# Kernel tuning notes

Hardware: AMD Instinct MI355X
Metric: run time of the kernel (lower is better)

The kernel has to match this reference:

```python
import jax, jax.numpy as jnp
import numpy as np

N, DIM, NH, HD, M = 2048, 1024, 16, 64, 2
LN_EPS = 1e-5


def setup_inputs() -> dict:
    key = jax.random.key(0)
    ks = jax.random.split(key, 8)
    x = jax.random.normal(ks[0], (N, DIM), dtype=jnp.float32)
    ids = jax.random.randint(ks[1], (N,), 0, M)
    modality_masks = jnp.stack([ids == m for m in range(M)])  # [M, N] bool partition
    s = 0.02
    wq = jax.random.normal(ks[2], (M, DIM, NH * HD), dtype=jnp.float32) * s
    wk = jax.random.normal(ks[3], (M, DIM, NH * HD), dtype=jnp.float32) * s
    wv = jax.random.normal(ks[4], (M, DIM, NH * HD), dtype=jnp.float32) * s
    wo = jax.random.normal(ks[5], (M, NH * HD, DIM), dtype=jnp.float32) * s
    ln_w = jnp.ones((M, DIM), dtype=jnp.float32)
    ln_b = jnp.zeros((M, DIM), dtype=jnp.float32)
    return dict(x=x, modality_masks=modality_masks, n_heads=NH,
                wq=wq, wk=wk, wv=wv, wo=wo, ln_w=ln_w, ln_b=ln_b)


def reference(x, modality_masks, n_heads, wq, wk, wv, wo, ln_w, ln_b):
    # x: [N, dim]; modality_masks: [M, N] bool (partition of tokens)
    n_mod, n_tok = modality_masks.shape
    hd = wq.shape[-1] // n_heads
    scale = hd ** -0.5

    mod_id = jnp.argmax(modality_masks, axis=0)          # [N] modality of each token
    perm = jnp.argsort(mod_id, stable=True)              # concat order: mod-0 tokens, then mod-1, ...
    xp = x[perm]                                          # gathered tokens in expert order
    oh = jax.nn.one_hot(mod_id[perm], n_mod, dtype=x.dtype)  # [N, M] expert selector

    def expert_proj(inp, w):
        # inp: [N, din], w: [M, din, dout] -> per-token output using that token's expert
        all_out = jnp.einsum('nd,mdo->mno', inp, w)       # [M, N, dout]
        return jnp.einsum('nm,mno->no', oh, all_out)      # select expert per token

    q = expert_proj(xp, wq).reshape(n_tok, n_heads, hd).transpose(1, 0, 2)  # [H, N, hd]
    k = expert_proj(xp, wk).reshape(n_tok, n_heads, hd).transpose(1, 0, 2)
    v = expert_proj(xp, wv).reshape(n_tok, n_heads, hd).transpose(1, 0, 2)

    scores = jnp.einsum('hnd,hkd->hnk', q, k) * scale     # [H, N, N] full attention over merged tokens
    probs = jax.nn.softmax(scores, axis=-1)
    attn = jnp.einsum('hnk,hkd->hnd', probs, v)           # [H, N, hd]
    attn = attn.transpose(1, 0, 2).reshape(n_tok, n_heads * hd)

    o = expert_proj(attn, wo)                              # [N, dim] per-modality wo
    mu = jnp.mean(o, axis=-1, keepdims=True)
    var = jnp.mean((o - mu) ** 2, axis=-1, keepdims=True)
    on = (o - mu) * jax.lax.rsqrt(var + LN_EPS)
    g = oh @ ln_w                                          # [N, dim] per-token LN scale
    b = oh @ ln_b
    out_perm = on * g + b

    out = jnp.zeros_like(x).at[perm].set(out_perm)         # scatter back to original order
    return out
```

## Files before the change

### kernel.cpp

```cpp
#include <hip/hip_runtime.h>

typedef __attribute__((ext_vector_type(8))) short short8v;
typedef __attribute__((ext_vector_type(4))) float f32x4;
typedef __attribute__((ext_vector_type(16))) float f32x16;
typedef unsigned short u16;
typedef unsigned int u32;

#define MFMA __builtin_amdgcn_mfma_f32_16x16x32_bf16
#define MFMA32 __builtin_amdgcn_mfma_f32_32x32x16_bf16

__device__ __forceinline__ u16 f2b(float f) {
  u32 u = __float_as_uint(f);
  u = (u + 0x7FFFu + ((u >> 16) & 1u)) >> 16;
  return (u16)u;
}
__device__ __forceinline__ void g2l16(const void* g, void* l) {
  __builtin_amdgcn_global_load_lds(
      (const __attribute__((address_space(1))) unsigned int*)g,
      (__attribute__((address_space(3))) unsigned int*)l, 16, 0, 0);
}

#define N_TOK 2048
#define DIM 1024
#define NH 16
#define HD 64

#define QSCALE 0.18033688011112042f

#define OFF_PERM 0
#define OFF_CNT 8192
#define OFF_XPB 16384
#define OFF_WT (OFF_XPB + 4194304)
#define OFF_Q (OFF_WT + 16777216)
#define OFF_K (OFF_Q + 4194304)
#define OFF_VT (OFF_K + 4194304)
#define OFF_AT (OFF_VT + 4194304)
#define OFF_O (OFF_AT + 4194304)
#define OFF_O2 (OFF_O + 8388608)

__global__ __launch_bounds__(256) void wcast_prep(const float* __restrict__ wq,
                                                  const float* __restrict__ wk,
                                                  const float* __restrict__ wv,
                                                  const float* __restrict__ wo,
                                                  u16* __restrict__ wT,
                                                  const void* __restrict__ masks,
                                                  int* __restrict__ perm,
                                                  int* __restrict__ cnt) {
  __shared__ float t[32][33];
  __shared__ u32 red[256];
  __shared__ int scan[256];
  const int tx = threadIdx.x, ty = threadIdx.y;
  if (blockIdx.z == 8) {
    if (blockIdx.x != 0 || blockIdx.y != 0) return;
    const int tid = ty * 32 + tx;
    const u32* mw = (const u32*)masks;
    u32 mx = 0;
    for (int i = tid; i < 1024; i += 256) { u32 v = mw[i]; mx = mx > v ? mx : v; }
    red[tid] = mx;
    __syncthreads();
    for (int off = 128; off; off >>= 1) {
      if (tid < off) red[tid] = red[tid] > red[tid + off] ? red[tid] : red[tid + off];
      __syncthreads();
    }
    const bool isbyte = red[0] > 1u;
    int md[8];
    int c0loc = 0;
    #pragma unroll
    for (int j = 0; j < 8; ++j) {
      const int n = tid * 8 + j;
      int m1;
      if (isbyte) m1 = ((const unsigned char*)masks)[N_TOK + n] != 0;
      else        m1 = mw[N_TOK + n] != 0;
      md[j] = m1;
      c0loc += (m1 == 0);
    }
    scan[tid] = c0loc;
    __syncthreads();
    for (int off = 1; off < 256; off <<= 1) {
      int v = (tid >= off) ? scan[tid - off] : 0;
      __syncthreads();
      scan[tid] += v;
      __syncthreads();
    }
    const int incl = scan[tid];
    const int total0 = scan[255];
    const int excl0 = incl - c0loc;
    int p0 = excl0;
    int p1 = total0 + (tid * 8 - excl0);
    #pragma unroll
    for (int j = 0; j < 8; ++j) {
      const int n = tid * 8 + j;
      if (!md[j]) perm[p0++] = n; else perm[p1++] = n;
    }
    if (tid == 0) cnt[0] = total0;
    return;
  }
  const int mat = blockIdx.z;
  const int tensor = mat >> 1, expert = mat & 1;
  const float* src = (tensor == 0) ? wq : (tensor == 1) ? wk : (tensor == 2) ? wv : wo;
  src += (size_t)expert * (1 << 20);
  u16* dst = wT + ((size_t)mat << 20);
  const int k0 = blockIdx.x * 32, n0 = blockIdx.y * 32;
  #pragma unroll
  for (int r = 0; r < 4; ++r)
    t[ty + 8 * r][tx] = src[(size_t)(k0 + ty + 8 * r) * DIM + n0 + tx];
  __syncthreads();
  #pragma unroll
  for (int r = 0; r < 4; ++r)
    dst[(size_t)(n0 + ty + 8 * r) * DIM + k0 + tx] = f2b(t[tx][ty + 8 * r]);
}

__global__ __launch_bounds__(256) void gather_cast(const float* __restrict__ x,
                                                   const int* __restrict__ perm,
                                                   u16* __restrict__ xpb) {
  const int i = blockIdx.x;
  const int src = perm[i];
  const int tid = threadIdx.x;
  float4 v = ((const float4*)(x + (size_t)src * DIM))[tid];
  ushort4 o;
  o.x = f2b(v.x); o.y = f2b(v.y); o.z = f2b(v.z); o.w = f2b(v.w);
  ((ushort4*)(xpb + (size_t)i * DIM))[tid] = o;
}

__global__ __launch_bounds__(256) void gemm_qkv(const u16* __restrict__ X,
                                                const u16* __restrict__ WTall,
                                                float qscale,
                                                u16* __restrict__ oq,
                                                u16* __restrict__ ok,
                                                u16* __restrict__ vT,
                                                const int* __restrict__ cntp) {
  const int z = blockIdx.z;
  const int e = blockIdx.y >> 4;
  const int mt = blockIdx.y & 15;
  const int c0 = cntp[0];
  const int lo = e ? c0 : 0;
  const int hi = e ? N_TOK : c0;
  const int rb = mt * 128;
  if (rb >= hi || rb + 128 <= lo) return;
  const int cb = blockIdx.x * 128;
  const u16* W = WTall + ((size_t)(z * 2 + e) << 20);
  const float scl = (z == 0) ? qscale : 1.f;

  const int tid = threadIdx.x;
  const int w = tid >> 6, l = tid & 63, lg = l >> 4, ln = l & 15;
  const int wm = (w >> 1) * 64, wn = (w & 1) * 64;

  __shared__ __align__(16) char smem[65536];

  auto stage = [&](int it, int b_) {
    #pragma unroll
    for (int c = 0; c < 8; ++c) {
      const int j = tid + c * 256;
      const int isB = j >> 10;
      const int cc = j & 1023;
      const int row = cc >> 3;
      const int colb = ((cc & 7) * 16) ^ ((row & 7) << 4);
      const char* base = isB ? (const char*)W + (size_t)(cb + row) * 2048
                             : (const char*)X + (size_t)(rb + row) * 2048;
      g2l16(base + it * 128 + colb, &smem[b_ * 32768 + isB * 16384 + cc * 16]);
    }
  };

  f32x4 acc[4][4];
  #pragma unroll
  for (int i = 0; i < 4; ++i)
    #pragma unroll
    for (int j = 0; j < 4; ++j) acc[i][j] = (f32x4){0.f, 0.f, 0.f, 0.f};

  const int aswz = (ln & 7) << 4;
  stage(0, 0);
  __syncthreads();
  for (int ii = 0; ii < 16; ++ii) {
    const int b_ = ii & 1;
    if (ii < 15) stage(ii + 1, b_ ^ 1);
    #pragma unroll
    for (int ks = 0; ks < 2; ++ks) {
      short8v a[4], bb[4];
      #pragma unroll
      for (int mi = 0; mi < 4; ++mi)
        a[mi] = *(const short8v*)&smem[b_ * 32768 + (wm + mi * 16 + ln) * 128 +
                                       ((ks * 64 + lg * 16) ^ aswz)];
      #pragma unroll
      for (int ni = 0; ni < 4; ++ni)
        bb[ni] = *(const short8v*)&smem[b_ * 32768 + 16384 + (wn + ni * 16 + ln) * 128 +
                                        ((ks * 64 + lg * 16) ^ aswz)];
      __builtin_amdgcn_s_setprio(1);
      #pragma unroll
      for (int mi = 0; mi < 4; ++mi)
        #pragma unroll
        for (int ni = 0; ni < 4; ++ni)
          acc[mi][ni] = MFMA(a[mi], bb[ni], acc[mi][ni], 0, 0, 0);
      __builtin_amdgcn_s_setprio(0);
    }
    __syncthreads();
  }

  if (z < 2) {
    u16* OUT = z ? ok : oq;
    #pragma unroll
    for (int mi = 0; mi < 4; ++mi) {
      #pragma unroll
      for (int r = 0; r < 4; ++r) {
        const int row = rb + wm + mi * 16 + lg * 4 + r;
        if (row >= lo && row < hi) {
          #pragma unroll
          for (int ni = 0; ni < 4; ++ni)
            OUT[(size_t)row * DIM + cb + wn + ni * 16 + ln] = f2b(acc[mi][ni][r] * scl);
        }
      }
    }
  } else {
    #pragma unroll
    for (int mi = 0; mi < 4; ++mi)
      #pragma unroll
      for (int ni = 0; ni < 4; ++ni) {
        const int dim = wn + ni * 16 + ln;
        const int tok = wm + mi * 16 + lg * 4;
        u32 p01, p23;
        asm("v_cvt_pk_bf16_f32 %0, %1, %2" : "=v"(p01) : "v"(acc[mi][ni][0]), "v"(acc[mi][ni][1]));
        asm("v_cvt_pk_bf16_f32 %0, %1, %2" : "=v"(p23) : "v"(acc[mi][ni][2]), "v"(acc[mi][ni][3]));
        *(uint2*)&smem[dim * 264 + tok * 2] = make_uint2(p01, p23);
      }
    __syncthreads();
    #pragma unroll 4
    for (int rr = 0; rr < 32; ++rr) {
      const int dim = w * 32 + rr;
      const u32 val = *(const u32*)&smem[dim * 264 + l * 4];
      const int tok = rb + 2 * l;
      u16* dst = vT + (size_t)(cb + dim) * 2048 + tok;
      if (tok >= lo && tok + 2 <= hi) {
        *(u32*)dst = val;
      } else {
        if (tok >= lo && tok < hi) dst[0] = (u16)(val & 0xFFFFu);
        if (tok + 1 >= lo && tok + 1 < hi) dst[1] = (u16)(val >> 16);
      }
    }
  }
}

__global__ __launch_bounds__(256) void gemm_out(const u16* __restrict__ X,
                                                const u16* __restrict__ WTall,
                                                float* __restrict__ o0,
                                                float* __restrict__ o1,
                                                const int* __restrict__ cntp) {
  const int z = blockIdx.z;
  const int e = blockIdx.y >> 4;
  const int mt = blockIdx.y & 15;
  const int c0 = cntp[0];
  const int lo = e ? c0 : 0;
  const int hi = e ? N_TOK : c0;
  const int rb = mt * 128;
  if (rb >= hi || rb + 128 <= lo) return;
  const int cb = blockIdx.x * 64;
  float* OUT = z ? o1 : o0;
  const u16* W = WTall + ((size_t)(6 + e) << 20);
  const int kstart = z * 8;

  const int tid = threadIdx.x;
  const int w = tid >> 6, l = tid & 63, lg = l >> 4, ln = l & 15;
  const int wm = w * 32;

  __shared__ __align__(16) char smem[49152];

  auto stage = [&](int it, int b_) {
    #pragma unroll
    for (int c = 0; c < 6; ++c) {
      const int j = tid + c * 256;
      const int isB = j >= 1024;
      const int cc = isB ? (j - 1024) : j;
      const int row = cc >> 3;
      const int colb = ((cc & 7) * 16) ^ ((row & 7) << 4);
      const char* base = isB ? (const char*)W + (size_t)(cb + row) * 2048
                             : (const char*)X + (size_t)(rb + row) * 2048;
      g2l16(base + it * 128 + colb, &smem[b_ * 24576 + isB * 16384 + cc * 16]);
    }
  };

  f32x4 acc[2][4];
  #pragma unroll
  for (int i = 0; i < 2; ++i)
    #pragma unroll
    for (int j = 0; j < 4; ++j) acc[i][j] = (f32x4){0.f, 0.f, 0.f, 0.f};

  const int aswz = (ln & 7) << 4;
  stage(kstart, 0);
  __syncthreads();
  for (int ii = 0; ii < 8; ++ii) {
    const int b_ = ii & 1;
    if (ii < 7) stage(kstart + ii + 1, b_ ^ 1);
    #pragma unroll
    for (int ks = 0; ks < 2; ++ks) {
      short8v a[2], bb[4];
      #pragma unroll
      for (int mi = 0; mi < 2; ++mi)
        a[mi] = *(const short8v*)&smem[b_ * 24576 + (wm + mi * 16 + ln) * 128 +
                                       ((ks * 64 + lg * 16) ^ aswz)];
      #pragma unroll
      for (int ni = 0; ni < 4; ++ni)
        bb[ni] = *(const short8v*)&smem[b_ * 24576 + 16384 + (ni * 16 + ln) * 128 +
                                        ((ks * 64 + lg * 16) ^ aswz)];
      __builtin_amdgcn_s_setprio(1);
      #pragma unroll
      for (int mi = 0; mi < 2; ++mi)
        #pragma unroll
        for (int ni = 0; ni < 4; ++ni)
          acc[mi][ni] = MFMA(a[mi], bb[ni], acc[mi][ni], 0, 0, 0);
      __builtin_amdgcn_s_setprio(0);
    }
    __syncthreads();
  }

  #pragma unroll
  for (int mi = 0; mi < 2; ++mi) {
    #pragma unroll
    for (int r = 0; r < 4; ++r) {
      const int row = rb + wm + mi * 16 + lg * 4 + r;
      if (row >= lo && row < hi) {
        #pragma unroll
        for (int ni = 0; ni < 4; ++ni)
          OUT[(size_t)row * DIM + cb + ni * 16 + ln] = acc[mi][ni][r];
      }
    }
  }
}

__global__ __launch_bounds__(256, 2) void attn_fwd(const u16* __restrict__ qg,
                                                   const u16* __restrict__ kg,
                                                   const u16* __restrict__ vTg,
                                                   u16* __restrict__ og) {
  const int bid = blockIdx.x;
  const int wg = (bid & 7) * 64 + (bid >> 3);
  const int qt = wg & 31, h = wg >> 5;
  const int tid = threadIdx.x, kq = tid >> 6, l = tid & 63;
  const int q31 = l & 31, hi = l >> 5;
  const int hi16 = hi * 16, hi4 = hi * 4;

  __shared__ __align__(16) char smem[67584];
  const int base = kq * 16384;

  const int lr3 = l >> 3, lc3 = l & 7;
  const char* baseK = (const char*)kg + (size_t)(kq * 512 + lr3) * 2048 + h * 128 +
                      ((lc3 << 4) ^ (lr3 << 4));
  const int cpr = lc3 ^ lr3;
  const int dhalf = (cpr >> 2) & 1;
  const char* baseV = (const char*)vTg + (size_t)(h * 64 + lr3 + dhalf * 32) * 4096 +
                      kq * 1024 + ((cpr & 3) << 4);

  const char* qb0 = (const char*)qg + (size_t)(qt * 64 + q31) * 2048 + h * 128;
  short8v qfA[4], qfB[4];
  #pragma unroll
  for (int t = 0; t < 4; ++t) {
    qfA[t] = *(const short8v*)(qb0 + t * 32 + hi16);
    qfB[t] = *(const short8v*)(qb0 + 65536 + t * 32 + hi16);
  }

  uint4 rk0, rk1, rk2, rk3, rv0, rv1, rv2, rv3;
  auto loadKV = [&](int it) {
    const char* pk = baseK + (size_t)it * 65536;
    rk0 = *(const uint4*)(pk);
    rk1 = *(const uint4*)(pk + 16384);
    rk2 = *(const uint4*)(pk + 32768);
    rk3 = *(const uint4*)(pk + 49152);
    const char* pv = baseV + it * 64;
    rv0 = *(const uint4*)(pv);
    rv1 = *(const uint4*)(pv + 32768);
    rv2 = *(const uint4*)(pv + 65536);
    rv3 = *(const uint4*)(pv + 98304);
  };
  auto writeK = [&](int b_) {
    const int Kb = base + b_ * 8192;
    *(uint4*)&smem[Kb + 0 + l * 16] = rk0;
    *(uint4*)&smem[Kb + 1024 + l * 16] = rk1;
    *(uint4*)&smem[Kb + 2048 + l * 16] = rk2;
    *(uint4*)&smem[Kb + 3072 + l * 16] = rk3;
  };
  auto writeV = [&](int b_) {
    const int Vb = base + b_ * 8192 + 4096;
    *(uint4*)&smem[Vb + 0 + l * 16] = rv0;
    *(uint4*)&smem[Vb + 1024 + l * 16] = rv1;
    *(uint4*)&smem[Vb + 2048 + l * 16] = rv2;
    *(uint4*)&smem[Vb + 3072 + l * 16] = rv3;
  };

  float mA = -1e30f, lA = 0.f, mB = -1e30f, lB = 0.f;
  f32x16 accA0, accA1, accB0, accB1;
  #pragma unroll
  for (int r = 0; r < 16; ++r) { accA0[r] = 0.f; accA1[r] = 0.f; accB0[r] = 0.f; accB1[r] = 0.f; }

  struct PA { short8v p0, p1; };
  auto softmax = [&](f32x16& s_, float& m_s, float& l_s, f32x16& a0, f32x16& a1) -> PA {
    float t0 = fmaxf(fmaxf(s_[0], s_[1]), fmaxf(s_[2], s_[3]));
    float t1 = fmaxf(fmaxf(s_[4], s_[5]), fmaxf(s_[6], s_[7]));
    float t2 = fmaxf(fmaxf(s_[8], s_[9]), fmaxf(s_[10], s_[11]));
    float t3 = fmaxf(fmaxf(s_[12], s_[13]), fmaxf(s_[14], s_[15]));
    float tmax = fmaxf(fmaxf(t0, t1), fmaxf(t2, t3));
    tmax = fmaxf(tmax, __shfl_xor(tmax, 32, 64));
    if (!__all(tmax <= m_s + 11.0f)) {
      const float mn = fmaxf(m_s, tmax);
      const float al = __builtin_amdgcn_exp2f(m_s - mn);
      m_s = mn;
      l_s *= al;
      #pragma unroll
      for (int r = 0; r < 16; ++r) {
        const float ar = __shfl(al, (r & 3) + 8 * (r >> 2) + hi4, 64);
        a0[r] *= ar;
        a1[r] *= ar;
      }
    }
    float p[16];
    #pragma unroll
    for (int r = 0; r < 16; ++r) p[r] = __builtin_amdgcn_exp2f(s_[r] - m_s);
    float rs = ((p[0] + p[1]) + (p[2] + p[3])) + ((p[4] + p[5]) + (p[6] + p[7])) +
               (((p[8] + p[9]) + (p[10] + p[11])) + ((p[12] + p[13]) + (p[14] + p[15])));
    rs += __shfl_xor(rs, 32, 64);
    l_s += rs;
    u32 c0, c1, c2, c3, c4, c5, c6, c7;
    asm("v_cvt_pk_bf16_f32 %0, %1, %2" : "=v"(c0) : "v"(p[0]), "v"(p[1]));
    asm("v_cvt_pk_bf16_f32 %0, %1, %2" : "=v"(c1) : "v"(p[2]), "v"(p[3]));
    asm("v_cvt_pk_bf16_f32 %0, %1, %2" : "=v"(c2) : "v"(p[4]), "v"(p[5]));
    asm("v_cvt_pk_bf16_f32 %0, %1, %2" : "=v"(c3) : "v"(p[6]), "v"(p[7]));
    asm("v_cvt_pk_bf16_f32 %0, %1, %2" : "=v"(c4) : "v"(p[8]), "v"(p[9]));
    asm("v_cvt_pk_bf16_f32 %0, %1, %2" : "=v"(c5) : "v"(p[10]), "v"(p[11]));
    asm("v_cvt_pk_bf16_f32 %0, %1, %2" : "=v"(c6) : "v"(p[12]), "v"(p[13]));
    asm("v_cvt_pk_bf16_f32 %0, %1, %2" : "=v"(c7) : "v"(p[14]), "v"(p[15]));
    asm volatile("v_permlane32_swap_b32 %0, %1" : "+v"(c0), "+v"(c2));
    asm volatile("v_permlane32_swap_b32 %0, %1" : "+v"(c1), "+v"(c3));
    asm volatile("v_permlane32_swap_b32 %0, %1" : "+v"(c4), "+v"(c6));
    asm volatile("v_permlane32_swap_b32 %0, %1" : "+v"(c5), "+v"(c7));
    union { u32 u[4]; short8v s; } u0, u1;
    u0.u[0] = c0; u0.u[1] = c1; u0.u[2] = c2; u0.u[3] = c3;
    u1.u[0] = c4; u1.u[1] = c5; u1.u[2] = c6; u1.u[3] = c7;
    PA out;
    out.p0 = u0.s;
    out.p1 = u1.s;
    return out;
  };

  const int kswz = (q31 & 7) << 4;
  loadKV(0);
  writeK(0);
  writeV(0);
  loadKV(1);

  #pragma unroll 1
  for (int it = 0; it < 16; ++it) {
    const int cur = it & 1, nxt = cur ^ 1;
    const int Kb = base + cur * 8192, Vb = Kb + 4096;
    short8v kf0 = *(const short8v*)&smem[Kb + q31 * 128 + ((0 + hi16) ^ kswz)];
    short8v kf1 = *(const short8v*)&smem[Kb + q31 * 128 + ((32 + hi16) ^ kswz)];
    short8v kf2 = *(const short8v*)&smem[Kb + q31 * 128 + ((64 + hi16) ^ kswz)];
    short8v kf3 = *(const short8v*)&smem[Kb + q31 * 128 + ((96 + hi16) ^ kswz)];
    f32x16 sA, sB;
    #pragma unroll
    for (int r = 0; r < 16; ++r) { sA[r] = 0.f; sB[r] = 0.f; }
    __builtin_amdgcn_s_setprio(1);
    sA = MFMA32(kf0, qfA[0], sA, 0, 0, 0);
    sB = MFMA32(kf0, qfB[0], sB, 0, 0, 0);
    sA = MFMA32(kf1, qfA[1], sA, 0, 0, 0);
    sB = MFMA32(kf1, qfB[1], sB, 0, 0, 0);
    sA = MFMA32(kf2, qfA[2], sA, 0, 0, 0);
    sB = MFMA32(kf2, qfB[2], sB, 0, 0, 0);
    sA = MFMA32(kf3, qfA[3], sA, 0, 0, 0);
    sB = MFMA32(kf3, qfB[3], sB, 0, 0, 0);
    __builtin_amdgcn_s_setprio(0);
    if (it < 15) writeK(nxt);

    PA pA = softmax(sA, mA, lA, accA0, accA1);
    PA pB = softmax(sB, mB, lB, accB0, accB1);

    short8v vf00 = *(const short8v*)&smem[Vb + q31 * 128 + ((0 + hi16) ^ kswz)];
    short8v vf01 = *(const short8v*)&smem[Vb + q31 * 128 + ((64 + hi16) ^ kswz)];
    short8v vf10 = *(const short8v*)&smem[Vb + q31 * 128 + ((32 + hi16) ^ kswz)];
    short8v vf11 = *(const short8v*)&smem[Vb + q31 * 128 + ((96 + hi16) ^ kswz)];
    __builtin_amdgcn_s_setprio(1);
    accA0 = MFMA32(pA.p0, vf00, accA0, 0, 0, 0);
    accA1 = MFMA32(pA.p0, vf01, accA1, 0, 0, 0);
    accB0 = MFMA32(pB.p0, vf00, accB0, 0, 0, 0);
    accB1 = MFMA32(pB.p0, vf01, accB1, 0, 0, 0);
    accA0 = MFMA32(pA.p1, vf10, accA0, 0, 0, 0);
    accA1 = MFMA32(pA.p1, vf11, accA1, 0, 0, 0);
    accB0 = MFMA32(pB.p1, vf10, accB0, 0, 0, 0);
    accB1 = MFMA32(pB.p1, vf11, accB1, 0, 0, 0);
    __builtin_amdgcn_s_setprio(0);
    if (it < 15) writeV(nxt);
    if (it < 14) loadKV(it + 2);
  }
  __syncthreads();

  float* mm = (float*)&smem[65536];
  if (l < 32) {
    mm[(0 * 4 + kq) * 32 + l] = mA;
    mm[(1 * 4 + kq) * 32 + l] = mB;
    mm[256 + (0 * 4 + kq) * 32 + l] = lA;
    mm[256 + (1 * 4 + kq) * 32 + l] = lB;
  }
  __syncthreads();
  float MA = mm[0 * 32 + q31], MB = mm[4 * 32 + q31];
  #pragma unroll
  for (int j = 1; j < 4; ++j) {
    MA = fmaxf(MA, mm[(0 * 4 + j) * 32 + q31]);
    MB = fmaxf(MB, mm[(1 * 4 + j) * 32 + q31]);
  }
  float LA = 0.f, LB = 0.f;
  #pragma unroll
  for (int j = 0; j < 4; ++j) {
    LA += mm[256 + (0 * 4 + j) * 32 + q31] * __builtin_amdgcn_exp2f(mm[(0 * 4 + j) * 32 + q31] - MA);
    LB += mm[256 + (1 * 4 + j) * 32 + q31] * __builtin_amdgcn_exp2f(mm[(1 * 4 + j) * 32 + q31] - MB);
  }
  const float aA = __builtin_amdgcn_exp2f(mA - MA), liA = 1.f / LA;
  const float aB = __builtin_amdgcn_exp2f(mB - MB), liB = 1.f / LB;

  float* obuf = (float*)&smem[0];
  #pragma unroll
  for (int round = 3; round >= 0; --round) {
    if (kq == round) {
      #pragma unroll
      for (int r = 0; r < 16; ++r) {
        const int qr = (r & 3) + 8 * (r >> 2) + hi4;
        const float arA = __shfl(aA, qr, 64);
        const float arB = __shfl(aB, qr, 64);
        float* pa0 = &obuf[qr * 64 + q31];
        float* pa1 = &obuf[qr * 64 + 32 + q31];
        float* pb0 = &obuf[(32 + qr) * 64 + q31];
        float* pb1 = &obuf[(32 + qr) * 64 + 32 + q31];
        if (round == 3) {
          *pa0 = accA0[r] * arA; *pa1 = accA1[r] * arA;
          *pb0 = accB0[r] * arB; *pb1 = accB1[r] * arB;
        } else if (round > 0) {
          *pa0 += accA0[r] * arA; *pa1 += accA1[r] * arA;
          *pb0 += accB0[r] * arB; *pb1 += accB1[r] * arB;
        } else {
          const float lrA = __shfl(liA, qr, 64);
          const float lrB = __shfl(liB, qr, 64);
          const int rowA = qt * 64 + qr, rowB = qt * 64 + 32 + qr;
          og[(size_t)rowA * DIM + h * HD + q31] = f2b((accA0[r] * arA + *pa0) * lrA);
          og[(size_t)rowA * DIM + h * HD + 32 + q31] = f2b((accA1[r] * arA + *pa1) * lrA);
          og[(size_t)rowB * DIM + h * HD + q31] = f2b((accB0[r] * arB + *pb0) * lrB);
          og[(size_t)rowB * DIM + h * HD + 32 + q31] = f2b((accB1[r] * arB + *pb1) * lrB);
        }
      }
    }
    __syncthreads();
  }
}

__global__ __launch_bounds__(256) void ln_scatter(const float* __restrict__ oa,
                                                  const float* __restrict__ ob,
                                                  const float* __restrict__ lnw,
                                                  const float* __restrict__ lnb,
                                                  const int* __restrict__ perm,
                                                  const int* __restrict__ cntp,
                                                  float* __restrict__ out) {
  const int i = blockIdx.x;
  const int tid = threadIdx.x, w = tid >> 6, l = tid & 63;
  const int mod = (i < cntp[0]) ? 0 : 1;
  float4 va = ((const float4*)(oa + (size_t)i * DIM))[tid];
  float4 vb = ((const float4*)(ob + (size_t)i * DIM))[tid];
  float4 v;
  v.x = va.x + vb.x; v.y = va.y + vb.y; v.z = va.z + vb.z; v.w = va.w + vb.w;
  float s = v.x + v.y + v.z + v.w;
  float ss = v.x * v.x + v.y * v.y + v.z * v.z + v.w * v.w;
  #pragma unroll
  for (int off = 1; off < 64; off <<= 1) {
    s += __shfl_xor(s, off, 64);
    ss += __shfl_xor(ss, off, 64);
  }
  __shared__ float rs4[4], rss4[4];
  if (l == 0) { rs4[w] = s; rss4[w] = ss; }
  __syncthreads();
  const float st = rs4[0] + rs4[1] + rs4[2] + rs4[3];
  const float sst = rss4[0] + rss4[1] + rss4[2] + rss4[3];
  const float mu = st * (1.f / DIM);
  const float var = sst * (1.f / DIM) - mu * mu;
  const float rstd = rsqrtf(var + 1e-5f);
  const int drow = perm[i];
  float4 g = ((const float4*)(lnw + (size_t)mod * DIM))[tid];
  float4 b = ((const float4*)(lnb + (size_t)mod * DIM))[tid];
  float4 rr;
  rr.x = (v.x - mu) * rstd * g.x + b.x;
  rr.y = (v.y - mu) * rstd * g.y + b.y;
  rr.z = (v.z - mu) * rstd * g.z + b.z;
  rr.w = (v.w - mu) * rstd * g.w + b.w;
  ((float4*)(out + (size_t)drow * DIM))[tid] = rr;
}

extern "C" void kernel_launch(void* const* d_in, const int* in_sizes, int n_in,
                              void* d_out, int out_size, void* d_ws, size_t ws_size,
                              hipStream_t stream) {
  const float* x = (const float*)d_in[0];
  const void* masks = d_in[1];
  const float* wq = (const float*)d_in[3];
  const float* wk = (const float*)d_in[4];
  const float* wv = (const float*)d_in[5];
  const float* wo = (const float*)d_in[6];
  const float* lnw = (const float*)d_in[7];
  const float* lnb = (const float*)d_in[8];

  char* ws = (char*)d_ws;
  int* perm = (int*)(ws + OFF_PERM);
  int* cnt = (int*)(ws + OFF_CNT);
  u16* xpb = (u16*)(ws + OFF_XPB);
  u16* wT = (u16*)(ws + OFF_WT);
  u16* q = (u16*)(ws + OFF_Q);
  u16* k = (u16*)(ws + OFF_K);
  u16* vT = (u16*)(ws + OFF_VT);
  u16* at = (u16*)(ws + OFF_AT);
  float* o = (float*)(ws + OFF_O);
  float* o2 = (float*)(ws + OFF_O2);
  float* out = (float*)d_out;

  wcast_prep<<<dim3(32, 32, 9), dim3(32, 8), 0, stream>>>(wq, wk, wv, wo, wT, masks, perm, cnt);
  gather_cast<<<N_TOK, 256, 0, stream>>>(x, perm, xpb);
  gemm_qkv<<<dim3(8, 32, 3), 256, 0, stream>>>(xpb, wT, QSCALE, q, k, vT, cnt);
  attn_fwd<<<512, 256, 0, stream>>>(q, k, vT, at);
  gemm_out<<<dim3(16, 32, 2), 256, 0, stream>>>(at, wT, o, o2, cnt);
  ln_scatter<<<N_TOK, 256, 0, stream>>>(o, o2, lnw, lnb, perm, cnt, out);
}
```

Before: 91.06 us.

## Fuse token gather and bf16 cast into QKV GEMM, vectorize weight cast, pair softmax

Drops the separate gather_cast kernel. The QKV GEMM now loads fp32 rows of x through perm into registers, converts them with packed bf16 conversion and writes them into swizzled LDS, while B is still staged with direct-to-LDS loads. This removes one launch and a 4 MB intermediate round trip, at the cost of more register pressure and reading the fp32 x once per column tile. The weight transpose-cast now writes packed 32-bit bf16 pairs, and the attention softmax for the two query blocks is merged into one routine that shares a single rescale vote.

Measured after the change: 112.3 us. +23.3%, slower.

```diff
diff --git a/kernel.cpp b/kernel.cpp
--- a/kernel.cpp
+++ b/kernel.cpp
@@ -29,8 +29,7 @@
 
 #define OFF_PERM 0
 #define OFF_CNT 8192
-#define OFF_XPB 16384
-#define OFF_WT (OFF_XPB + 4194304)
+#define OFF_WT 16384
 #define OFF_Q (OFF_WT + 16777216)
 #define OFF_K (OFF_Q + 4194304)
 #define OFF_VT (OFF_K + 4194304)
@@ -105,24 +104,21 @@
   for (int r = 0; r < 4; ++r)
     t[ty + 8 * r][tx] = src[(size_t)(k0 + ty + 8 * r) * DIM + n0 + tx];
   __syncthreads();
-  #pragma unroll
-  for (int r = 0; r < 4; ++r)
-    dst[(size_t)(n0 + ty + 8 * r) * DIM + k0 + tx] = f2b(t[tx][ty + 8 * r]);
-}
-
-__global__ __launch_bounds__(256) void gather_cast(const float* __restrict__ x,
-                                                   const int* __restrict__ perm,
-                                                   u16* __restrict__ xpb) {
-  const int i = blockIdx.x;
-  const int src = perm[i];
-  const int tid = threadIdx.x;
-  float4 v = ((const float4*)(x + (size_t)src * DIM))[tid];
-  ushort4 o;
-  o.x = f2b(v.x); o.y = f2b(v.y); o.z = f2b(v.z); o.w = f2b(v.w);
-  ((ushort4*)(xpb + (size_t)i * DIM))[tid] = o;
-}
-
-__global__ __launch_bounds__(256) void gemm_qkv(const u16* __restrict__ X,
+  const int tid = ty * 32 + tx;
+  const int row = tid >> 3, pr = tid & 7;
+  u32* dst32 = (u32*)(dst + (size_t)(n0 + row) * DIM + k0);
+  #pragma unroll
+  for (int j = 0; j < 2; ++j) {
+    const int kp = pr + j * 8;
+    u32 val;
+    asm("v_cvt_pk_bf16_f32 %0, %1, %2" : "=v"(val)
+        : "v"(t[2 * kp][row]), "v"(t[2 * kp + 1][row]));
+    dst32[kp] = val;
+  }
+}
+
+__global__ __launch_bounds__(256) void gemm_qkv(const float* __restrict__ x,
+                                                const int* __restrict__ perm,
                                                 const u16* __restrict__ WTall,
                                                 float qscale,
                                                 u16* __restrict__ oq,
@@ -147,17 +143,36 @@
 
   __shared__ __align__(16) char smem[65536];
 
-  auto stage = [&](int it, int b_) {
-    #pragma unroll
-    for (int c = 0; c < 8; ++c) {
-      const int j = tid + c * 256;
-      const int isB = j >> 10;
-      const int cc = j & 1023;
+  const int arow = tid >> 1, ahalf = tid & 1;
+  const float* apx = x + (size_t)perm[rb + arow] * DIM + ahalf * 32;
+  float4 af[8];
+  auto loadA = [&](int it) {
+    const float4* p = (const float4*)(apx + it * 64);
+    #pragma unroll
+    for (int j = 0; j < 8; ++j) af[j] = p[j];
+  };
+  auto writeA = [&](int b_) {
+    #pragma unroll
+    for (int j16 = 0; j16 < 4; ++j16) {
+      u32 pk0, pk1, pk2, pk3;
+      const float4 f0 = af[j16 * 2], f1 = af[j16 * 2 + 1];
+      asm("v_cvt_pk_bf16_f32 %0, %1, %2" : "=v"(pk0) : "v"(f0.x), "v"(f0.y));
+      asm("v_cvt_pk_bf16_f32 %0, %1, %2" : "=v"(pk1) : "v"(f0.z), "v"(f0.w));
+      asm("v_cvt_pk_bf16_f32 %0, %1, %2" : "=v"(pk2) : "v"(f1.x), "v"(f1.y));
+      asm("v_cvt_pk_bf16_f32 %0, %1, %2" : "=v"(pk3) : "v"(f1.z), "v"(f1.w));
+      *(uint4*)&smem[b_ * 32768 + arow * 128 +
+                     ((ahalf * 64 + j16 * 16) ^ ((arow & 7) << 4))] =
+          make_uint4(pk0, pk1, pk2, pk3);
+    }
+  };
+  auto stageB = [&](int it, int b_) {
+    #pragma unroll
+    for (int c = 0; c < 4; ++c) {
+      const int cc = tid + c * 256;
       const int row = cc >> 3;
       const int colb = ((cc & 7) * 16) ^ ((row & 7) << 4);
-      const char* base = isB ? (const char*)W + (size_t)(cb + row) * 2048
-                             : (const char*)X + (size_t)(rb + row) * 2048;
-      g2l16(base + it * 128 + colb, &smem[b_ * 32768 + isB * 16384 + cc * 16]);
+      g2l16((const char*)W + (size_t)(cb + row) * 2048 + it * 128 + colb,
+            &smem[b_ * 32768 + 16384 + cc * 16]);
     }
   };
 
@@ -168,11 +183,13 @@
     for (int j = 0; j < 4; ++j) acc[i][j] = (f32x4){0.f, 0.f, 0.f, 0.f};
 
   const int aswz = (ln & 7) << 4;
-  stage(0, 0);
+  loadA(0);
+  stageB(0, 0);
+  writeA(0);
   __syncthreads();
   for (int ii = 0; ii < 16; ++ii) {
     const int b_ = ii & 1;
-    if (ii < 15) stage(ii + 1, b_ ^ 1);
+    if (ii < 15) { loadA(ii + 1); stageB(ii + 1, b_ ^ 1); }
     #pragma unroll
     for (int ks = 0; ks < 2; ++ks) {
       short8v a[4], bb[4];
@@ -192,6 +209,7 @@
           acc[mi][ni] = MFMA(a[mi], bb[ni], acc[mi][ni], 0, 0, 0);
       __builtin_amdgcn_s_setprio(0);
     }
+    if (ii < 15) writeA(b_ ^ 1);
     __syncthreads();
   }
 
@@ -388,52 +406,81 @@
   for (int r = 0; r < 16; ++r) { accA0[r] = 0.f; accA1[r] = 0.f; accB0[r] = 0.f; accB1[r] = 0.f; }
 
   struct PA { short8v p0, p1; };
-  auto softmax = [&](f32x16& s_, float& m_s, float& l_s, f32x16& a0, f32x16& a1) -> PA {
-    float t0 = fmaxf(fmaxf(s_[0], s_[1]), fmaxf(s_[2], s_[3]));
-    float t1 = fmaxf(fmaxf(s_[4], s_[5]), fmaxf(s_[6], s_[7]));
-    float t2 = fmaxf(fmaxf(s_[8], s_[9]), fmaxf(s_[10], s_[11]));
-    float t3 = fmaxf(fmaxf(s_[12], s_[13]), fmaxf(s_[14], s_[15]));
-    float tmax = fmaxf(fmaxf(t0, t1), fmaxf(t2, t3));
-    tmax = fmaxf(tmax, __shfl_xor(tmax, 32, 64));
-    if (!__all(tmax <= m_s + 11.0f)) {
-      const float mn = fmaxf(m_s, tmax);
-      const float al = __builtin_amdgcn_exp2f(m_s - mn);
-      m_s = mn;
-      l_s *= al;
+
+  auto softmax_pair = [&](f32x16& sA_, f32x16& sB_, PA& oA, PA& oB) {
+    float tA0 = fmaxf(fmaxf(sA_[0], sA_[1]), fmaxf(sA_[2], sA_[3]));
+    float tB0 = fmaxf(fmaxf(sB_[0], sB_[1]), fmaxf(sB_[2], sB_[3]));
+    float tA1 = fmaxf(fmaxf(sA_[4], sA_[5]), fmaxf(sA_[6], sA_[7]));
+    float tB1 = fmaxf(fmaxf(sB_[4], sB_[5]), fmaxf(sB_[6], sB_[7]));
+    float tA2 = fmaxf(fmaxf(sA_[8], sA_[9]), fmaxf(sA_[10], sA_[11]));
+    float tB2 = fmaxf(fmaxf(sB_[8], sB_[9]), fmaxf(sB_[10], sB_[11]));
+    float tA3 = fmaxf(fmaxf(sA_[12], sA_[13]), fmaxf(sA_[14], sA_[15]));
+    float tB3 = fmaxf(fmaxf(sB_[12], sB_[13]), fmaxf(sB_[14], sB_[15]));
+    float tmA = fmaxf(fmaxf(tA0, tA1), fmaxf(tA2, tA3));
+    float tmB = fmaxf(fmaxf(tB0, tB1), fmaxf(tB2, tB3));
+    tmA = fmaxf(tmA, __shfl_xor(tmA, 32, 64));
+    tmB = fmaxf(tmB, __shfl_xor(tmB, 32, 64));
+    const bool okb = (tmA <= mA + 11.0f) && (tmB <= mB + 11.0f);
+    if (!__all(okb)) {
+      const float mnA = fmaxf(mA, tmA), mnB = fmaxf(mB, tmB);
+      const float alA = __builtin_amdgcn_exp2f(mA - mnA);
+      const float alB = __builtin_amdgcn_exp2f(mB - mnB);
+      mA = mnA; mB = mnB; lA *= alA; lB *= alB;
       #pragma unroll
       for (int r = 0; r < 16; ++r) {
-        const float ar = __shfl(al, (r & 3) + 8 * (r >> 2) + hi4, 64);
-        a0[r] *= ar;
-        a1[r] *= ar;
+        const int qr = (r & 3) + 8 * (r >> 2) + hi4;
+        const float arA = __shfl(alA, qr, 64);
+        const float arB = __shfl(alB, qr, 64);
+        accA0[r] *= arA; accA1[r] *= arA;
+        accB0[r] *= arB; accB1[r] *= arB;
       }
     }
-    float p[16];
-    #pragma unroll
-    for (int r = 0; r < 16; ++r) p[r] = __builtin_amdgcn_exp2f(s_[r] - m_s);
-    float rs = ((p[0] + p[1]) + (p[2] + p[3])) + ((p[4] + p[5]) + (p[6] + p[7])) +
-               (((p[8] + p[9]) + (p[10] + p[11])) + ((p[12] + p[13]) + (p[14] + p[15])));
-    rs += __shfl_xor(rs, 32, 64);
-    l_s += rs;
-    u32 c0, c1, c2, c3, c4, c5, c6, c7;
-    asm("v_cvt_pk_bf16_f32 %0, %1, %2" : "=v"(c0) : "v"(p[0]), "v"(p[1]));
-    asm("v_cvt_pk_bf16_f32 %0, %1, %2" : "=v"(c1) : "v"(p[2]), "v"(p[3]));
-    asm("v_cvt_pk_bf16_f32 %0, %1, %2" : "=v"(c2) : "v"(p[4]), "v"(p[5]));
-    asm("v_cvt_pk_bf16_f32 %0, %1, %2" : "=v"(c3) : "v"(p[6]), "v"(p[7]));
-    asm("v_cvt_pk_bf16_f32 %0, %1, %2" : "=v"(c4) : "v"(p[8]), "v"(p[9]));
-    asm("v_cvt_pk_bf16_f32 %0, %1, %2" : "=v"(c5) : "v"(p[10]), "v"(p[11]));
-    asm("v_cvt_pk_bf16_f32 %0, %1, %2" : "=v"(c6) : "v"(p[12]), "v"(p[13]));
-    asm("v_cvt_pk_bf16_f32 %0, %1, %2" : "=v"(c7) : "v"(p[14]), "v"(p[15]));
-    asm volatile("v_permlane32_swap_b32 %0, %1" : "+v"(c0), "+v"(c2));
-    asm volatile("v_permlane32_swap_b32 %0, %1" : "+v"(c1), "+v"(c3));
-    asm volatile("v_permlane32_swap_b32 %0, %1" : "+v"(c4), "+v"(c6));
-    asm volatile("v_permlane32_swap_b32 %0, %1" : "+v"(c5), "+v"(c7));
-    union { u32 u[4]; short8v s; } u0, u1;
-    u0.u[0] = c0; u0.u[1] = c1; u0.u[2] = c2; u0.u[3] = c3;
-    u1.u[0] = c4; u1.u[1] = c5; u1.u[2] = c6; u1.u[3] = c7;
-    PA out;
-    out.p0 = u0.s;
-    out.p1 = u1.s;
-    return out;
+    float pA_[16], pB_[16];
+    #pragma unroll
+    for (int r = 0; r < 16; ++r) {
+      pA_[r] = __builtin_amdgcn_exp2f(sA_[r] - mA);
+      pB_[r] = __builtin_amdgcn_exp2f(sB_[r] - mB);
+    }
+    float rsA = ((pA_[0] + pA_[1]) + (pA_[2] + pA_[3])) + ((pA_[4] + pA_[5]) + (pA_[6] + pA_[7])) +
+                (((pA_[8] + pA_[9]) + (pA_[10] + pA_[11])) + ((pA_[12] + pA_[13]) + (pA_[14] + pA_[15])));
+    float rsB = ((pB_[0] + pB_[1]) + (pB_[2] + pB_[3])) + ((pB_[4] + pB_[5]) + (pB_[6] + pB_[7])) +
+                (((pB_[8] + pB_[9]) + (pB_[10] + pB_[11])) + ((pB_[12] + pB_[13]) + (pB_[14] + pB_[15])));
+    rsA += __shfl_xor(rsA, 32, 64);
+    rsB += __shfl_xor(rsB, 32, 64);
+    lA += rsA;
+    lB += rsB;
+    u32 a0, a1, a2, a3, a4, a5, a6, a7, b0, b1, b2, b3, b4, b5, b6, b7;
+    asm("v_cvt_pk_bf16_f32 %0, %1, %2" : "=v"(a0) : "v"(pA_[0]), "v"(pA_[1]));
+    asm("v_cvt_pk_bf16_f32 %0, %1, %2" : "=v"(a1) : "v"(pA_[2]), "v"(pA_[3]));
+    asm("v_cvt_pk_bf16_f32 %0, %1, %2" : "=v"(a2) : "v"(pA_[4]), "v"(pA_[5]));
+    asm("v_cvt_pk_bf16_f32 %0, %1, %2" : "=v"(a3) : "v"(pA_[6]), "v"(pA_[7]));
+    asm("v_cvt_pk_bf16_f32 %0, %1, %2" : "=v"(a4) : "v"(pA_[8]), "v"(pA_[9]));
+    asm("v_cvt_pk_bf16_f32 %0, %1, %2" : "=v"(a5) : "v"(pA_[10]), "v"(pA_[11]));
+    asm("v_cvt_pk_bf16_f32 %0, %1, %2" : "=v"(a6) : "v"(pA_[12]), "v"(pA_[13]));
+    asm("v_cvt_pk_bf16_f32 %0, %1, %2" : "=v"(a7) : "v"(pA_[14]), "v"(pA_[15]));
+    asm("v_cvt_pk_bf16_f32 %0, %1, %2" : "=v"(b0) : "v"(pB_[0]), "v"(pB_[1]));
+    asm("v_cvt_pk_bf16_f32 %0, %1, %2" : "=v"(b1) : "v"(pB_[2]), "v"(pB_[3]));
+    asm("v_cvt_pk_bf16_f32 %0, %1, %2" : "=v"(b2) : "v"(pB_[4]), "v"(pB_[5]));
+    asm("v_cvt_pk_bf16_f32 %0, %1, %2" : "=v"(b3) : "v"(pB_[6]), "v"(pB_[7]));
+    asm("v_cvt_pk_bf16_f32 %0, %1, %2" : "=v"(b4) : "v"(pB_[8]), "v"(pB_[9]));
+    asm("v_cvt_pk_bf16_f32 %0, %1, %2" : "=v"(b5) : "v"(pB_[10]), "v"(pB_[11]));
+    asm("v_cvt_pk_bf16_f32 %0, %1, %2" : "=v"(b6) : "v"(pB_[12]), "v"(pB_[13]));
+    asm("v_cvt_pk_bf16_f32 %0, %1, %2" : "=v"(b7) : "v"(pB_[14]), "v"(pB_[15]));
+    asm volatile("v_permlane32_swap_b32 %0, %1" : "+v"(a0), "+v"(a2));
+    asm volatile("v_permlane32_swap_b32 %0, %1" : "+v"(a1), "+v"(a3));
+    asm volatile("v_permlane32_swap_b32 %0, %1" : "+v"(a4), "+v"(a6));
+    asm volatile("v_permlane32_swap_b32 %0, %1" : "+v"(a5), "+v"(a7));
+    asm volatile("v_permlane32_swap_b32 %0, %1" : "+v"(b0), "+v"(b2));
+    asm volatile("v_permlane32_swap_b32 %0, %1" : "+v"(b1), "+v"(b3));
+    asm volatile("v_permlane32_swap_b32 %0, %1" : "+v"(b4), "+v"(b6));
+    asm volatile("v_permlane32_swap_b32 %0, %1" : "+v"(b5), "+v"(b7));
+    union { u32 u[4]; short8v s; } uA0, uA1, uB0, uB1;
+    uA0.u[0] = a0; uA0.u[1] = a1; uA0.u[2] = a2; uA0.u[3] = a3;
+    uA1.u[0] = a4; uA1.u[1] = a5; uA1.u[2] = a6; uA1.u[3] = a7;
+    uB0.u[0] = b0; uB0.u[1] = b1; uB0.u[2] = b2; uB0.u[3] = b3;
+    uB1.u[0] = b4; uB1.u[1] = b5; uB1.u[2] = b6; uB1.u[3] = b7;
+    oA.p0 = uA0.s; oA.p1 = uA1.s;
+    oB.p0 = uB0.s; oB.p1 = uB1.s;
   };
 
   const int kswz = (q31 & 7) << 4;
@@ -465,8 +512,8 @@
     __builtin_amdgcn_s_setprio(0);
     if (it < 15) writeK(nxt);
 
-    PA pA = softmax(sA, mA, lA, accA0, accA1);
-    PA pB = softmax(sB, mB, lB, accB0, accB1);
+    PA pA, pB;
+    softmax_pair(sA, sB, pA, pB);
 
     short8v vf00 = *(const short8v*)&smem[Vb + q31 * 128 + ((0 + hi16) ^ kswz)];
     short8v vf01 = *(const short8v*)&smem[Vb + q31 * 128 + ((64 + hi16) ^ kswz)];
@@ -599,7 +646,6 @@
   char* ws = (char*)d_ws;
   int* perm = (int*)(ws + OFF_PERM);
   int* cnt = (int*)(ws + OFF_CNT);
-  u16* xpb = (u16*)(ws + OFF_XPB);
   u16* wT = (u16*)(ws + OFF_WT);
   u16* q = (u16*)(ws + OFF_Q);
   u16* k = (u16*)(ws + OFF_K);
@@ -610,8 +656,7 @@
   float* out = (float*)d_out;
 
   wcast_prep<<<dim3(32, 32, 9), dim3(32, 8), 0, stream>>>(wq, wk, wv, wo, wT, masks, perm, cnt);
-  gather_cast<<<N_TOK, 256, 0, stream>>>(x, perm, xpb);
-  gemm_qkv<<<dim3(8, 32, 3), 256, 0, stream>>>(xpb, wT, QSCALE, q, k, vT, cnt);
+  gemm_qkv<<<dim3(8, 32, 3), 256, 0, stream>>>(x, perm, wT, QSCALE, q, k, vT, cnt);
   attn_fwd<<<512, 256, 0, stream>>>(q, k, vT, at);
   gemm_out<<<dim3(16, 32, 2), 256, 0, stream>>>(at, wT, o, o2, cnt);
   ln_scatter<<<N_TOK, 256, 0, stream>>>(o, o2, lnw, lnb, perm, cnt, out);
```

## Split attention work across eight waves and pack bf16 weight-transpose stores

Applied to the files above, without the earlier changes.

The attention kernel moves from 4 waves per block, each handling 64 query rows over a KV quarter, to 8 waves per block. Each wave now handles 32 query rows over a KV quarter, with a single wave-private LDS buffer instead of a double buffer. The aim is more wave-level parallelism and fewer live accumulators per wave. In exchange, the two waves sharing a KV quarter load the same K/V data twice. The launch bound of 4 blocks of 512 threads may also force a tight VGPR cap and cause spills, and LDS size likely allows only 2 blocks per CU anyway. Separately, the weight transpose/cast now writes packed 32-bit bf16 pairs using v_cvt_pk_bf16_f32 instead of scalar 16-bit stores.

Measured after the change: 96.02 us. +5.4%, slower.

```diff
diff --git a/kernel.cpp b/kernel.cpp
--- a/kernel.cpp
+++ b/kernel.cpp
@@ -105,9 +105,17 @@
   for (int r = 0; r < 4; ++r)
     t[ty + 8 * r][tx] = src[(size_t)(k0 + ty + 8 * r) * DIM + n0 + tx];
   __syncthreads();
-  #pragma unroll
-  for (int r = 0; r < 4; ++r)
-    dst[(size_t)(n0 + ty + 8 * r) * DIM + k0 + tx] = f2b(t[tx][ty + 8 * r]);
+  const int tid = ty * 32 + tx;
+  const int row = tid >> 3, pr = tid & 7;
+  u32* dst32 = (u32*)(dst + (size_t)(n0 + row) * DIM + k0);
+  #pragma unroll
+  for (int j = 0; j < 2; ++j) {
+    const int kp = pr + j * 8;
+    u32 val;
+    asm("v_cvt_pk_bf16_f32 %0, %1, %2" : "=v"(val)
+        : "v"(t[2 * kp][row]), "v"(t[2 * kp + 1][row]));
+    dst32[kp] = val;
+  }
 }
 
 __global__ __launch_bounds__(256) void gather_cast(const float* __restrict__ x,
@@ -324,19 +332,20 @@
   }
 }
 
-__global__ __launch_bounds__(256, 2) void attn_fwd(const u16* __restrict__ qg,
+__global__ __launch_bounds__(512, 4) void attn_fwd(const u16* __restrict__ qg,
                                                    const u16* __restrict__ kg,
                                                    const u16* __restrict__ vTg,
                                                    u16* __restrict__ og) {
   const int bid = blockIdx.x;
   const int wg = (bid & 7) * 64 + (bid >> 3);
   const int qt = wg & 31, h = wg >> 5;
-  const int tid = threadIdx.x, kq = tid >> 6, l = tid & 63;
+  const int tid = threadIdx.x, w = tid >> 6, l = tid & 63;
+  const int g = w & 1, kq = w >> 1;
   const int q31 = l & 31, hi = l >> 5;
   const int hi16 = hi * 16, hi4 = hi * 4;
 
   __shared__ __align__(16) char smem[67584];
-  const int base = kq * 16384;
+  const int Kb = w * 8192, Vb = Kb + 4096;
 
   const int lr3 = l >> 3, lc3 = l & 7;
   const char* baseK = (const char*)kg + (size_t)(kq * 512 + lr3) * 2048 + h * 128 +
@@ -346,13 +355,10 @@
   const char* baseV = (const char*)vTg + (size_t)(h * 64 + lr3 + dhalf * 32) * 4096 +
                       kq * 1024 + ((cpr & 3) << 4);
 
-  const char* qb0 = (const char*)qg + (size_t)(qt * 64 + q31) * 2048 + h * 128;
-  short8v qfA[4], qfB[4];
-  #pragma unroll
-  for (int t = 0; t < 4; ++t) {
-    qfA[t] = *(const short8v*)(qb0 + t * 32 + hi16);
-    qfB[t] = *(const short8v*)(qb0 + 65536 + t * 32 + hi16);
-  }
+  const char* qb0 = (const char*)qg + (size_t)(qt * 64 + g * 32 + q31) * 2048 + h * 128;
+  short8v qf[4];
+  #pragma unroll
+  for (int t = 0; t < 4; ++t) qf[t] = *(const short8v*)(qb0 + t * 32 + hi16);
 
   uint4 rk0, rk1, rk2, rk3, rv0, rv1, rv2, rv3;
   auto loadKV = [&](int it) {
@@ -367,28 +373,47 @@
     rv2 = *(const uint4*)(pv + 65536);
     rv3 = *(const uint4*)(pv + 98304);
   };
-  auto writeK = [&](int b_) {
-    const int Kb = base + b_ * 8192;
+  auto writeK = [&]() {
     *(uint4*)&smem[Kb + 0 + l * 16] = rk0;
     *(uint4*)&smem[Kb + 1024 + l * 16] = rk1;
     *(uint4*)&smem[Kb + 2048 + l * 16] = rk2;
     *(uint4*)&smem[Kb + 3072 + l * 16] = rk3;
   };
-  auto writeV = [&](int b_) {
-    const int Vb = base + b_ * 8192 + 4096;
+  auto writeV = [&]() {
     *(uint4*)&smem[Vb + 0 + l * 16] = rv0;
     *(uint4*)&smem[Vb + 1024 + l * 16] = rv1;
     *(uint4*)&smem[Vb + 2048 + l * 16] = rv2;
     *(uint4*)&smem[Vb + 3072 + l * 16] = rv3;
   };
 
-  float mA = -1e30f, lA = 0.f, mB = -1e30f, lB = 0.f;
-  f32x16 accA0, accA1, accB0, accB1;
-  #pragma unroll
-  for (int r = 0; r < 16; ++r) { accA0[r] = 0.f; accA1[r] = 0.f; accB0[r] = 0.f; accB1[r] = 0.f; }
-
-  struct PA { short8v p0, p1; };
-  auto softmax = [&](f32x16& s_, float& m_s, float& l_s, f32x16& a0, f32x16& a1) -> PA {
+  float m_s = -1e30f, l_s = 0.f;
+  f32x16 acc0, acc1;
+  #pragma unroll
+  for (int r = 0; r < 16; ++r) { acc0[r] = 0.f; acc1[r] = 0.f; }
+
+  const int kswz = (q31 & 7) << 4;
+  loadKV(0);
+  writeK();
+  writeV();
+  loadKV(1);
+
+  #pragma unroll 1
+  for (int it = 0; it < 16; ++it) {
+    short8v kf0 = *(const short8v*)&smem[Kb + q31 * 128 + ((0 + hi16) ^ kswz)];
+    short8v kf1 = *(const short8v*)&smem[Kb + q31 * 128 + ((32 + hi16) ^ kswz)];
+    short8v kf2 = *(const short8v*)&smem[Kb + q31 * 128 + ((64 + hi16) ^ kswz)];
+    short8v kf3 = *(const short8v*)&smem[Kb + q31 * 128 + ((96 + hi16) ^ kswz)];
+    if (it < 15) writeK();
+    f32x16 s_;
+    #pragma unroll
+    for (int r = 0; r < 16; ++r) s_[r] = 0.f;
+    __builtin_amdgcn_s_setprio(1);
+    s_ = MFMA32(kf0, qf[0], s_, 0, 0, 0);
+    s_ = MFMA32(kf1, qf[1], s_, 0, 0, 0);
+    s_ = MFMA32(kf2, qf[2], s_, 0, 0, 0);
+    s_ = MFMA32(kf3, qf[3], s_, 0, 0, 0);
+    __builtin_amdgcn_s_setprio(0);
+
     float t0 = fmaxf(fmaxf(s_[0], s_[1]), fmaxf(s_[2], s_[3]));
     float t1 = fmaxf(fmaxf(s_[4], s_[5]), fmaxf(s_[6], s_[7]));
     float t2 = fmaxf(fmaxf(s_[8], s_[9]), fmaxf(s_[10], s_[11]));
@@ -403,8 +428,8 @@
       #pragma unroll
       for (int r = 0; r < 16; ++r) {
         const float ar = __shfl(al, (r & 3) + 8 * (r >> 2) + hi4, 64);
-        a0[r] *= ar;
-        a1[r] *= ar;
+        acc0[r] *= ar;
+        acc1[r] *= ar;
       }
     }
     float p[16];
@@ -414,6 +439,7 @@
                (((p[8] + p[9]) + (p[10] + p[11])) + ((p[12] + p[13]) + (p[14] + p[15])));
     rs += __shfl_xor(rs, 32, 64);
     l_s += rs;
+
     u32 c0, c1, c2, c3, c4, c5, c6, c7;
     asm("v_cvt_pk_bf16_f32 %0, %1, %2" : "=v"(c0) : "v"(p[0]), "v"(p[1]));
     asm("v_cvt_pk_bf16_f32 %0, %1, %2" : "=v"(c1) : "v"(p[2]), "v"(p[3]));
@@ -427,116 +453,64 @@
     asm volatile("v_permlane32_swap_b32 %0, %1" : "+v"(c1), "+v"(c3));
     asm volatile("v_permlane32_swap_b32 %0, %1" : "+v"(c4), "+v"(c6));
     asm volatile("v_permlane32_swap_b32 %0, %1" : "+v"(c5), "+v"(c7));
-    union { u32 u[4]; short8v s; } u0, u1;
-    u0.u[0] = c0; u0.u[1] = c1; u0.u[2] = c2; u0.u[3] = c3;
-    u1.u[0] = c4; u1.u[1] = c5; u1.u[2] = c6; u1.u[3] = c7;
-    PA out;
-    out.p0 = u0.s;
-    out.p1 = u1.s;
-    return out;
-  };
-
-  const int kswz = (q31 & 7) << 4;
-  loadKV(0);
-  writeK(0);
-  writeV(0);
-  loadKV(1);
-
-  #pragma unroll 1
-  for (int it = 0; it < 16; ++it) {
-    const int cur = it & 1, nxt = cur ^ 1;
-    const int Kb = base + cur * 8192, Vb = Kb + 4096;
-    short8v kf0 = *(const short8v*)&smem[Kb + q31 * 128 + ((0 + hi16) ^ kswz)];
-    short8v kf1 = *(const short8v*)&smem[Kb + q31 * 128 + ((32 + hi16) ^ kswz)];
-    short8v kf2 = *(const short8v*)&smem[Kb + q31 * 128 + ((64 + hi16) ^ kswz)];
-    short8v kf3 = *(const short8v*)&smem[Kb + q31 * 128 + ((96 + hi16) ^ kswz)];
-    f32x16 sA, sB;
-    #pragma unroll
-    for (int r = 0; r < 16; ++r) { sA[r] = 0.f; sB[r] = 0.f; }
-    __builtin_amdgcn_s_setprio(1);
-    sA = MFMA32(kf0, qfA[0], sA, 0, 0, 0);
-    sB = MFMA32(kf0, qfB[0], sB, 0, 0, 0);
-    sA = MFMA32(kf1, qfA[1], sA, 0, 0, 0);
-    sB = MFMA32(kf1, qfB[1], sB, 0, 0, 0);
-    sA = MFMA32(kf2, qfA[2], sA, 0, 0, 0);
-    sB = MFMA32(kf2, qfB[2], sB, 0, 0, 0);
-    sA = MFMA32(kf3, qfA[3], sA, 0, 0, 0);
-    sB = MFMA32(kf3, qfB[3], sB, 0, 0, 0);
-    __builtin_amdgcn_s_setprio(0);
-    if (it < 15) writeK(nxt);
-
-    PA pA = softmax(sA, mA, lA, accA0, accA1);
-    PA pB = softmax(sB, mB, lB, accB0, accB1);
+    union { u32 u[4]; short8v s; } pa0, pa1;
+    pa0.u[0] = c0; pa0.u[1] = c1; pa0.u[2] = c2; pa0.u[3] = c3;
+    pa1.u[0] = c4; pa1.u[1] = c5; pa1.u[2] = c6; pa1.u[3] = c7;
 
     short8v vf00 = *(const short8v*)&smem[Vb + q31 * 128 + ((0 + hi16) ^ kswz)];
     short8v vf01 = *(const short8v*)&smem[Vb + q31 * 128 + ((64 + hi16) ^ kswz)];
     short8v vf10 = *(const short8v*)&smem[Vb + q31 * 128 + ((32 + hi16) ^ kswz)];
     short8v vf11 = *(const short8v*)&smem[Vb + q31 * 128 + ((96 + hi16) ^ kswz)];
+    if (it < 15) writeV();
     __builtin_amdgcn_s_setprio(1);
-    accA0 = MFMA32(pA.p0, vf00, accA0, 0, 0, 0);
-    accA1 = MFMA32(pA.p0, vf01, accA1, 0, 0, 0);
-    accB0 = MFMA32(pB.p0, vf00, accB0, 0, 0, 0);
-    accB1 = MFMA32(pB.p0, vf01, accB1, 0, 0, 0);
-    accA0 = MFMA32(pA.p1, vf10, accA0, 0, 0, 0);
-    accA1 = MFMA32(pA.p1, vf11, accA1, 0, 0, 0);
-    accB0 = MFMA32(pB.p1, vf10, accB0, 0, 0, 0);
-    accB1 = MFMA32(pB.p1, vf11, accB1, 0, 0, 0);
+    acc0 = MFMA32(pa0.s, vf00, acc0, 0, 0, 0);
+    acc1 = MFMA32(pa0.s, vf01, acc1, 0, 0, 0);
+    acc0 = MFMA32(pa1.s, vf10, acc0, 0, 0, 0);
+    acc1 = MFMA32(pa1.s, vf11, acc1, 0, 0, 0);
     __builtin_amdgcn_s_setprio(0);
-    if (it < 15) writeV(nxt);
     if (it < 14) loadKV(it + 2);
   }
   __syncthreads();
 
   float* mm = (float*)&smem[65536];
   if (l < 32) {
-    mm[(0 * 4 + kq) * 32 + l] = mA;
-    mm[(1 * 4 + kq) * 32 + l] = mB;
-    mm[256 + (0 * 4 + kq) * 32 + l] = lA;
-    mm[256 + (1 * 4 + kq) * 32 + l] = lB;
+    mm[(g * 4 + kq) * 32 + l] = m_s;
+    mm[256 + (g * 4 + kq) * 32 + l] = l_s;
   }
   __syncthreads();
-  float MA = mm[0 * 32 + q31], MB = mm[4 * 32 + q31];
-  #pragma unroll
-  for (int j = 1; j < 4; ++j) {
-    MA = fmaxf(MA, mm[(0 * 4 + j) * 32 + q31]);
-    MB = fmaxf(MB, mm[(1 * 4 + j) * 32 + q31]);
-  }
-  float LA = 0.f, LB = 0.f;
-  #pragma unroll
-  for (int j = 0; j < 4; ++j) {
-    LA += mm[256 + (0 * 4 + j) * 32 + q31] * __builtin_amdgcn_exp2f(mm[(0 * 4 + j) * 32 + q31] - MA);
-    LB += mm[256 + (1 * 4 + j) * 32 + q31] * __builtin_amdgcn_exp2f(mm[(1 * 4 + j) * 32 + q31] - MB);
-  }
-  const float aA = __builtin_amdgcn_exp2f(mA - MA), liA = 1.f / LA;
-  const float aB = __builtin_amdgcn_exp2f(mB - MB), liB = 1.f / LB;
-
-  float* obuf = (float*)&smem[0];
+  float M = mm[(g * 4 + 0) * 32 + q31];
+  M = fmaxf(M, mm[(g * 4 + 1) * 32 + q31]);
+  M = fmaxf(M, mm[(g * 4 + 2) * 32 + q31]);
+  M = fmaxf(M, mm[(g * 4 + 3) * 32 + q31]);
+  float L = 0.f;
+  #pragma unroll
+  for (int j = 0; j < 4; ++j)
+    L += mm[256 + (g * 4 + j) * 32 + q31] *
+         __builtin_amdgcn_exp2f(mm[(g * 4 + j) * 32 + q31] - M);
+  const float aown = __builtin_amdgcn_exp2f(m_s - M);
+  const float linv = 1.f / L;
+
+  float* obuf = (float*)&smem[g * 8192];
   #pragma unroll
   for (int round = 3; round >= 0; --round) {
     if (kq == round) {
       #pragma unroll
       for (int r = 0; r < 16; ++r) {
         const int qr = (r & 3) + 8 * (r >> 2) + hi4;
-        const float arA = __shfl(aA, qr, 64);
-        const float arB = __shfl(aB, qr, 64);
-        float* pa0 = &obuf[qr * 64 + q31];
-        float* pa1 = &obuf[qr * 64 + 32 + q31];
-        float* pb0 = &obuf[(32 + qr) * 64 + q31];
-        float* pb1 = &obuf[(32 + qr) * 64 + 32 + q31];
+        const float ar = __shfl(aown, qr, 64);
+        float* p0 = &obuf[qr * 64 + q31];
+        float* p1 = &obuf[qr * 64 + 32 + q31];
         if (round == 3) {
-          *pa0 = accA0[r] * arA; *pa1 = accA1[r] * arA;
-          *pb0 = accB0[r] * arB; *pb1 = accB1[r] * arB;
+          *p0 = acc0[r] * ar;
+          *p1 = acc1[r] * ar;
         } else if (round > 0) {
-          *pa0 += accA0[r] * arA; *pa1 += accA1[r] * arA;
-          *pb0 += accB0[r] * arB; *pb1 += accB1[r] * arB;
+          *p0 += acc0[r] * ar;
+          *p1 += acc1[r] * ar;
         } else {
-          const float lrA = __shfl(liA, qr, 64);
-          const float lrB = __shfl(liB, qr, 64);
-          const int rowA = qt * 64 + qr, rowB = qt * 64 + 32 + qr;
-          og[(size_t)rowA * DIM + h * HD + q31] = f2b((accA0[r] * arA + *pa0) * lrA);
-          og[(size_t)rowA * DIM + h * HD + 32 + q31] = f2b((accA1[r] * arA + *pa1) * lrA);
-          og[(size_t)rowB * DIM + h * HD + q31] = f2b((accB0[r] * arB + *pb0) * lrB);
-          og[(size_t)rowB * DIM + h * HD + 32 + q31] = f2b((accB1[r] * arB + *pb1) * lrB);
+          const float li = __shfl(linv, qr, 64);
+          const int row = qt * 64 + g * 32 + qr;
+          og[(size_t)row * DIM + h * HD + q31] = f2b((acc0[r] * ar + *p0) * li);
+          og[(size_t)row * DIM + h * HD + 32 + q31] = f2b((acc1[r] * ar + *p1) * li);
         }
       }
     }
@@ -612,7 +586,7 @@
   wcast_prep<<<dim3(32, 32, 9), dim3(32, 8), 0, stream>>>(wq, wk, wv, wo, wT, masks, perm, cnt);
   gather_cast<<<N_TOK, 256, 0, stream>>>(x, perm, xpb);
   gemm_qkv<<<dim3(8, 32, 3), 256, 0, stream>>>(xpb, wT, QSCALE, q, k, vT, cnt);
-  attn_fwd<<<512, 256, 0, stream>>>(q, k, vT, at);
+  attn_fwd<<<512, 512, 0, stream>>>(q, k, vT, at);
   gemm_out<<<dim3(16, 32, 2), 256, 0, stream>>>(at, wT, o, o2, cnt);
   ln_scatter<<<N_TOK, 256, 0, stream>>>(o, o2, lnw, lnb, perm, cnt, out);
 }
```
